# Performance work log

Measured on AMD Instinct MI355X. Metric: run time of the kernel, lower is better.

## Reference

```python
import jax, jax.numpy as jnp
import numpy as np

N_NODES = 50000
N_EDGES = 1600000
IN_CH = 256
LAT = 32
HID = 64
OUT_CH = 256
GAT_H = 32  # GAT hidden dims [32, 32], heads=1


def setup_inputs() -> dict:
    key = jax.random.key(0)
    ks = jax.random.split(key, 30)
    nrm = lambda k, shape, s=0.05: jax.random.normal(k, shape, dtype=jnp.float32) * s
    inp = {}
    inp["x"] = jax.random.normal(ks[0], (N_NODES, IN_CH), dtype=jnp.float32)
    inp["edge_index"] = jax.random.randint(ks[1], (2, N_EDGES), 0, N_NODES)
    # GAT layer 1: IN_CH -> 32 (heads=1), layer 2: 32 -> 32, final linear 32 -> LAT
    inp["W_g1"] = nrm(ks[2], (IN_CH, GAT_H)); inp["as_g1"] = nrm(ks[3], (GAT_H,)); inp["ad_g1"] = nrm(ks[4], (GAT_H,)); inp["b_g1"] = jnp.zeros((GAT_H,), jnp.float32)
    inp["W_g2"] = nrm(ks[5], (GAT_H, GAT_H)); inp["as_g2"] = nrm(ks[6], (GAT_H,)); inp["ad_g2"] = nrm(ks[7], (GAT_H,)); inp["b_g2"] = jnp.zeros((GAT_H,), jnp.float32)
    inp["W_gf"] = nrm(ks[8], (GAT_H, LAT)); inp["b_gf"] = jnp.zeros((LAT,), jnp.float32)
    inp["W_m1"] = nrm(ks[9], (IN_CH, HID)); inp["b_m1"] = jnp.zeros((HID,), jnp.float32); inp["g_m1"] = jnp.ones((HID,), jnp.float32); inp["be_m1"] = jnp.zeros((HID,), jnp.float32)
    inp["W_m2"] = nrm(ks[10], (HID, HID)); inp["b_m2"] = jnp.zeros((HID,), jnp.float32); inp["g_m2"] = jnp.ones((HID,), jnp.float32); inp["be_m2"] = jnp.zeros((HID,), jnp.float32)
    inp["W_m3"] = nrm(ks[11], (HID, LAT)); inp["b_m3"] = jnp.zeros((LAT,), jnp.float32); inp["g_m3"] = jnp.ones((LAT,), jnp.float32); inp["be_m3"] = jnp.zeros((LAT,), jnp.float32)
    # final linear LAT -> OUT_CH + ReLU
    inp["W_f"] = nrm(ks[12], (LAT, OUT_CH)); inp["b_f"] = jnp.zeros((OUT_CH,), jnp.float32)
    return inp


def _bn_relu(h, g, b):
    # BatchNorm1d in training mode: batch stats, biased variance, eps=1e-5
    m = jnp.mean(h, axis=0)
    v = jnp.var(h, axis=0)
    return jax.nn.relu((h - m) * jax.lax.rsqrt(v + 1e-5) * g + b)


def _gat(h_in, src, dst, W, a_s, a_d, b):
    # PyG GATConv (heads=1): edge (src j -> dst i), e = LeakyReLU(a_src.Wx_j + a_dst.Wx_i)
    N = h_in.shape[0]
    h = h_in @ W                                   # [N, F]
    e = jax.nn.leaky_relu((h @ a_s)[src] + (h @ a_d)[dst], 0.2)  # [E]
    m = jax.ops.segment_max(e, dst, num_segments=N)              # scatter-softmax over incoming edges
    ex = jnp.exp(e - m[dst])
    den = jax.ops.segment_sum(ex, dst, num_segments=N)
    alpha = ex / den[dst]
    out = jax.ops.segment_sum(alpha[:, None] * h[src], dst, num_segments=N)
    return out + b


def reference(x, edge_index, W_g1, as_g1, ad_g1, b_g1, W_g2, as_g2, ad_g2, b_g2, W_gf, b_gf, W_m1, b_m1, g_m1, be_m1, W_m2, b_m2, g_m2, be_m2, W_m3, b_m3, g_m3, be_m3, W_f, b_f):
    N = x.shape[0]
    loops = jnp.arange(N)
    src = jnp.concatenate([edge_index[0], loops])  # PyG add_self_loops=True
    dst = jnp.concatenate([edge_index[1], loops])
    r = _bn_relu(x @ W_m1 + b_m1, g_m1, be_m1)
    r = _bn_relu(r @ W_m2 + b_m2, g_m2, be_m2)
    r = _bn_relu(r @ W_m3 + b_m3, g_m3, be_m3)
    # GAT interpolation branch (dropout inactive in eval)
    h = jax.nn.relu(_gat(x, src, dst, W_g1, as_g1, ad_g1, b_g1))
    h = jax.nn.relu(_gat(h, src, dst, W_g2, as_g2, ad_g2, b_g2))
    h = h @ W_gf + b_gf
    # blend with alphas = 0.5 constant vector
    out = 0.5 * r + 0.5 * h
    return jax.nn.relu(out @ W_f + b_f)
```

## Files before the change

kernel.cpp:

```cpp
#include <hip/hip_runtime.h>

#define NNODES 50000
#define NEDGES 1600000
#define NBUCK 196
#define BIN_CH 8192
#define CNT_CH 4096

__device__ __forceinline__ float leaky02(float x) { return x > 0.f ? x : 0.2f * x; }

__device__ __forceinline__ int block_incl_scan(int v, int* sh) {
  int t = threadIdx.x;
  sh[t] = v;
  __syncthreads();
  for (int d = 1; d < 256; d <<= 1) {
    int u = (t >= d) ? sh[t - d] : 0;
    __syncthreads();
    sh[t] += u;
    __syncthreads();
  }
  return sh[t];
}

__global__ __launch_bounds__(256) void k_b0(const int* __restrict__ dst,
                                            int* __restrict__ gcnt, int E) {
  __shared__ int hist[256];
  int t = threadIdx.x;
  hist[t] = 0;
  __syncthreads();
  int base0 = blockIdx.x * CNT_CH;
#pragma unroll
  for (int r = 0; r < CNT_CH / 256; ++r) {
    int idx = base0 + r * 256 + t;
    if (idx < E) atomicAdd(&hist[dst[idx] >> 8], 1);
  }
  __syncthreads();
  if (t < NBUCK && hist[t]) atomicAdd(&gcnt[t], hist[t]);
}

__global__ __launch_bounds__(256) void k_b1(const int* __restrict__ gcnt,
                                            int* __restrict__ base,
                                            int* __restrict__ cursor) {
  __shared__ int sh[256];
  int t = threadIdx.x;
  int v = (t < NBUCK) ? gcnt[t] : 0;
  int incl = block_incl_scan(v, sh);
  if (t < NBUCK) {
    base[t] = incl - v;
    cursor[t] = incl - v;
  }
  if (t == 255) base[NBUCK] = NEDGES;
}

__global__ __launch_bounds__(256) void k_bin(const int* __restrict__ src,
                                             const int* __restrict__ dst,
                                             int* __restrict__ cursor,
                                             unsigned* __restrict__ binned, int E) {
  __shared__ int hist[256];
  __shared__ int scanbuf[256];
  __shared__ int LS[NBUCK + 1];
  __shared__ int cur[256];
  __shared__ int gbase[256];
  __shared__ unsigned stage[BIN_CH];
  int t = threadIdx.x;
  int base0 = blockIdx.x * BIN_CH;
  int cnt = E - base0;
  if (cnt > BIN_CH) cnt = BIN_CH;

  unsigned pk[BIN_CH / 256];
  hist[t] = 0;
  __syncthreads();
#pragma unroll
  for (int r = 0; r < BIN_CH / 256; ++r) {
    int idx = base0 + r * 256 + t;
    if (idx < E) {
      unsigned p = ((unsigned)dst[idx] << 16) | (unsigned)src[idx];
      pk[r] = p;
      atomicAdd(&hist[p >> 24], 1);
    }
  }
  __syncthreads();
  int incl = block_incl_scan(hist[t], scanbuf);
  if (t == 0) LS[0] = 0;
  if (t < NBUCK) LS[t + 1] = incl;
  if (t < NBUCK && hist[t]) gbase[t] = atomicAdd(&cursor[t], hist[t]);
  __syncthreads();
  cur[t] = LS[t < NBUCK ? t : NBUCK];
  __syncthreads();
#pragma unroll
  for (int r = 0; r < BIN_CH / 256; ++r) {
    int idx = base0 + r * 256 + t;
    if (idx < E) {
      unsigned p = pk[r];
      int pos = atomicAdd(&cur[p >> 24], 1);
      stage[pos] = p;
    }
  }
  __syncthreads();
  for (int i = t; i < cnt; i += 256) {
    int lo = 0, hi = NBUCK;
    while (hi - lo > 1) {
      int mid = (lo + hi) >> 1;
      if (i >= LS[mid]) lo = mid; else hi = mid;
    }
    binned[gbase[lo] + (i - LS[lo])] = stage[i];
  }
}

__global__ __launch_bounds__(256) void k_sort(const unsigned* __restrict__ binned,
                                              const int* __restrict__ base,
                                              int* __restrict__ deg,
                                              int* __restrict__ offs,
                                              int* __restrict__ csr) {
  __shared__ int hist[256];
  __shared__ int scanbuf[256];
  __shared__ int cur[256];
  int t = threadIdx.x;
  int b = blockIdx.x;
  int lo = base[b], hi = base[b + 1];
  int node0 = b << 8;
  hist[t] = 0;
  __syncthreads();
  for (int i = lo + t; i < hi; i += 256)
    atomicAdd(&hist[(binned[i] >> 16) & 255], 1);
  __syncthreads();
  int h = hist[t];
  int incl = block_incl_scan(h, scanbuf);
  int excl = incl - h;
  int node = node0 + t;
  if (node < NNODES) {
    deg[node] = h;
    offs[node] = lo + excl;
  }
  cur[t] = lo + excl;
  __syncthreads();
  for (int i = lo + t; i < hi; i += 256) {
    unsigned p = binned[i];
    int pos = atomicAdd(&cur[(p >> 16) & 255], 1);
    csr[pos] = (int)(p & 0xFFFFu);
  }
}

template <int K, int KC, int NC, int TN, int SPLIT, bool BN, bool STATS>
__global__ __launch_bounds__(256) void k_gemm(
    const float* __restrict__ A, const float* __restrict__ scale,
    const float* __restrict__ shift, const float* __restrict__ B0,
    const float* __restrict__ B1, const float* __restrict__ bias0,
    float* __restrict__ out0, float* __restrict__ out1,
    float* __restrict__ gsum, float* __restrict__ gsq, int M) {
  __shared__ float As[128][68];
  __shared__ float Bs[KC][NC];
  const int tid = threadIdx.x;
  const int row0 = blockIdx.x * 128;
  const int cg = tid & 15;
  const int rowg = (tid >> 4) & 15;

  float acc[8][TN];
#pragma unroll
  for (int r = 0; r < 8; ++r)
#pragma unroll
    for (int j = 0; j < TN; ++j) acc[r][j] = 0.f;

  constexpr int KB = KC / 4;
  for (int k0 = 0; k0 < K; k0 += KC) {
#pragma unroll
    for (int it = 0; it < (128 * KB) / 256; ++it) {
      int idx = tid + it * 256;
      int row = idx / KB;
      int kb = idx % KB;
      float4 v = make_float4(0.f, 0.f, 0.f, 0.f);
      int grow = row0 + row;
      if (grow < M) {
        v = *reinterpret_cast<const float4*>(&A[(size_t)grow * K + k0 + kb * 4]);
        if (BN) {
          int kb4 = k0 + kb * 4;
          float4 sc = *reinterpret_cast<const float4*>(&scale[kb4]);
          float4 sf = *reinterpret_cast<const float4*>(&shift[kb4]);
          v.x = fmaxf(v.x * sc.x + sf.x, 0.f);
          v.y = fmaxf(v.y * sc.y + sf.y, 0.f);
          v.z = fmaxf(v.z * sc.z + sf.z, 0.f);
          v.w = fmaxf(v.w * sc.w + sf.w, 0.f);
        }
      }
      *reinterpret_cast<float4*>(&As[row][kb * 4]) = v;
    }
#pragma unroll
    for (int it = 0; it < (KC * SPLIT) / 256; ++it) {
      int idx = tid + it * 256;
      int kk = idx / SPLIT;
      int c = idx % SPLIT;
      Bs[kk][c] = B0[(size_t)(k0 + kk) * SPLIT + c];
    }
    if constexpr (NC > SPLIT) {
      constexpr int W1 = NC - SPLIT;
#pragma unroll
      for (int it = 0; it < (KC * W1) / 256; ++it) {
        int idx = tid + it * 256;
        int kk = idx / W1;
        int c = idx % W1;
        Bs[kk][SPLIT + c] = B1[(size_t)(k0 + kk) * W1 + c];
      }
    }
    __syncthreads();
    for (int kk = 0; kk < KC; kk += 4) {
      float4 a[8];
#pragma unroll
      for (int r = 0; r < 8; ++r)
        a[r] = *reinterpret_cast<const float4*>(&As[rowg + 16 * r][kk]);
      float b[4][TN];
#pragma unroll
      for (int i = 0; i < 4; ++i)
#pragma unroll
        for (int j = 0; j < TN; ++j) b[i][j] = Bs[kk + i][cg * TN + j];
#pragma unroll
      for (int r = 0; r < 8; ++r)
#pragma unroll
        for (int j = 0; j < TN; ++j) {
          acc[r][j] += a[r].x * b[0][j];
          acc[r][j] += a[r].y * b[1][j];
          acc[r][j] += a[r].z * b[2][j];
          acc[r][j] += a[r].w * b[3][j];
        }
    }
    __syncthreads();
  }
  float bias_r[TN];
#pragma unroll
  for (int j = 0; j < TN; ++j) {
    int c = cg * TN + j;
    bias_r[j] = (c < SPLIT) ? bias0[c] : 0.f;
  }
  float cs[TN], cq[TN];
#pragma unroll
  for (int j = 0; j < TN; ++j) { cs[j] = 0.f; cq[j] = 0.f; }
#pragma unroll
  for (int r = 0; r < 8; ++r) {
    int grow = row0 + rowg + 16 * r;
    if (grow < M) {
#pragma unroll
      for (int j = 0; j < TN; ++j) {
        int c = cg * TN + j;
        if (c < SPLIT) {
          float v = acc[r][j] + bias_r[j];
          out0[(size_t)grow * SPLIT + c] = v;
          if (STATS) { cs[j] += v; cq[j] += v * v; }
        } else {
          out1[(size_t)grow * (NC - SPLIT) + (c - SPLIT)] = acc[r][j];
        }
      }
    }
  }
  if constexpr (STATS) {
#pragma unroll
    for (int j = 0; j < TN; ++j) {
      cs[j] += __shfl_xor(cs[j], 16);
      cs[j] += __shfl_xor(cs[j], 32);
      cq[j] += __shfl_xor(cq[j], 16);
      cq[j] += __shfl_xor(cq[j], 32);
    }
    float* red = &Bs[0][0];
    int wave = tid >> 6;
    int lane = tid & 63;
    if (lane < 16) {
#pragma unroll
      for (int j = 0; j < TN; ++j) {
        int c = cg * TN + j;
        if (c < SPLIT) {
          red[wave * 2 * SPLIT + c] = cs[j];
          red[wave * 2 * SPLIT + SPLIT + c] = cq[j];
        }
      }
    }
    __syncthreads();
    if (tid < SPLIT) {
      float s = red[tid] + red[2 * SPLIT + tid] + red[4 * SPLIT + tid] + red[6 * SPLIT + tid];
      atomicAdd(&gsum[tid], s);
    } else if (tid < 2 * SPLIT) {
      int c = tid - SPLIT;
      float q = red[SPLIT + c] + red[3 * SPLIT + c] + red[5 * SPLIT + c] + red[7 * SPLIT + c];
      atomicAdd(&gsq[c], q);
    }
  }
}

__global__ __launch_bounds__(256) void k_sdot(const float* __restrict__ g,
                                              const float* __restrict__ as_,
                                              const float* __restrict__ ad_,
                                              float* __restrict__ sv,
                                              float* __restrict__ dv, int N) {
  int lane = threadIdx.x & 31;
  int row = blockIdx.x * 8 + (threadIdx.x >> 5);
  if (row >= N) return;
  float v = g[(size_t)row * 32 + lane];
  float a = v * as_[lane];
  float b = v * ad_[lane];
#pragma unroll
  for (int w = 16; w >= 1; w >>= 1) {
    a += __shfl_xor(a, w);
    b += __shfl_xor(b, w);
  }
  if (lane == 0) {
    sv[row] = a;
    dv[row] = b;
  }
}

__global__ __launch_bounds__(256) void k_gat_agg(
    const float* __restrict__ h, const float* __restrict__ sv,
    const float* __restrict__ dv, const int* __restrict__ offs,
    const int* __restrict__ deg, const int* __restrict__ csr,
    const float* __restrict__ bias, float* __restrict__ out, int N) {
  int lane = threadIdx.x & 31;
  int node = blockIdx.x * 8 + (threadIdx.x >> 5);
  if (node >= N) return;
  int start = offs[node];
  int cnt = deg[node];
  float di = dv[node];
  float ex0 = __expf(leaky02(sv[node] + di));
  float den = ex0;
  float acc = ex0 * h[(size_t)node * 32 + lane];
  int k = 0;
  for (; k + 8 <= cnt; k += 8) {
    int j0 = csr[start + k + 0], j1 = csr[start + k + 1];
    int j2 = csr[start + k + 2], j3 = csr[start + k + 3];
    int j4 = csr[start + k + 4], j5 = csr[start + k + 5];
    int j6 = csr[start + k + 6], j7 = csr[start + k + 7];
    float s0 = sv[j0], s1 = sv[j1], s2 = sv[j2], s3 = sv[j3];
    float s4 = sv[j4], s5 = sv[j5], s6 = sv[j6], s7 = sv[j7];
    float h0 = h[(size_t)j0 * 32 + lane], h1 = h[(size_t)j1 * 32 + lane];
    float h2 = h[(size_t)j2 * 32 + lane], h3 = h[(size_t)j3 * 32 + lane];
    float h4 = h[(size_t)j4 * 32 + lane], h5 = h[(size_t)j5 * 32 + lane];
    float h6 = h[(size_t)j6 * 32 + lane], h7 = h[(size_t)j7 * 32 + lane];
    float e0 = __expf(leaky02(s0 + di)), e1 = __expf(leaky02(s1 + di));
    float e2 = __expf(leaky02(s2 + di)), e3 = __expf(leaky02(s3 + di));
    float e4 = __expf(leaky02(s4 + di)), e5 = __expf(leaky02(s5 + di));
    float e6 = __expf(leaky02(s6 + di)), e7 = __expf(leaky02(s7 + di));
    den += ((e0 + e1) + (e2 + e3)) + ((e4 + e5) + (e6 + e7));
    acc += e0 * h0 + e1 * h1 + e2 * h2 + e3 * h3;
    acc += e4 * h4 + e5 * h5 + e6 * h6 + e7 * h7;
  }
  for (; k < cnt; ++k) {
    int j = csr[start + k];
    float ex = __expf(leaky02(sv[j] + di));
    den += ex;
    acc += ex * h[(size_t)j * 32 + lane];
  }
  out[(size_t)node * 32 + lane] = fmaxf(acc / den + bias[lane], 0.f);
}

__global__ __launch_bounds__(256) void k_small_gemm_sd(
    const float* __restrict__ hin, const float* __restrict__ W,
    const float* __restrict__ as_, const float* __restrict__ ad_,
    float* __restrict__ gout, float* __restrict__ sv, float* __restrict__ dv,
    int N) {
  __shared__ float Ws[32][32];
  {
    int t = threadIdx.x;
#pragma unroll
    for (int r = 0; r < 4; ++r) {
      int idx = t + r * 256;
      Ws[idx >> 5][idx & 31] = W[idx];
    }
  }
  __syncthreads();
  int lane = threadIdx.x & 31;
  int row = blockIdx.x * 8 + (threadIdx.x >> 5);
  if (row >= N) return;
  float hv = hin[(size_t)row * 32 + lane];
  float acc = 0.f;
#pragma unroll
  for (int k = 0; k < 32; ++k) acc += __shfl(hv, k, 32) * Ws[k][lane];
  gout[(size_t)row * 32 + lane] = acc;
  float a = acc * as_[lane];
  float b = acc * ad_[lane];
#pragma unroll
  for (int w = 16; w >= 1; w >>= 1) {
    a += __shfl_xor(a, w);
    b += __shfl_xor(b, w);
  }
  if (lane == 0) {
    sv[row] = a;
    dv[row] = b;
  }
}

__global__ void k_finalize(const float* __restrict__ sum, const float* __restrict__ sumsq,
                           const float* __restrict__ gamma, const float* __restrict__ beta,
                           float* __restrict__ scale, float* __restrict__ shift, int NC,
                           float invM) {
  int c = threadIdx.x;
  if (c < NC) {
    float mean = sum[c] * invM;
    float var = sumsq[c] * invM - mean * mean;
    float rs = rsqrtf(var + 1e-5f);
    float sc = rs * gamma[c];
    scale[c] = sc;
    shift[c] = beta[c] - mean * sc;
  }
}

__global__ __launch_bounds__(256) void k_final2(
    const float* __restrict__ mlp3, const float* __restrict__ sc3,
    const float* __restrict__ sh3, const float* __restrict__ h2,
    const float* __restrict__ Wgf, const float* __restrict__ bgf,
    const float* __restrict__ Wf, const float* __restrict__ bf,
    float* __restrict__ out, int N) {
  __shared__ float WfS[32 * 256];
  __shared__ float Bl[64][36];
  __shared__ float WgfS[32][33];
  __shared__ float colS[3][32];
  const int t = threadIdx.x;
  const int row0 = blockIdx.x * 64;

  {
    const float4* src = reinterpret_cast<const float4*>(Wf);
    float4* dst = reinterpret_cast<float4*>(WfS);
#pragma unroll
    for (int r = 0; r < 8; ++r) dst[t + r * 256] = src[t + r * 256];
  }
#pragma unroll
  for (int r = 0; r < 4; ++r) {
    int idx = t + r * 256;
    WgfS[idx >> 5][idx & 31] = Wgf[idx];
  }
  if (t < 32) {
    colS[0][t] = sc3[t];
    colS[1][t] = sh3[t];
    colS[2][t] = bgf[t];
  }
#pragma unroll
  for (int r = 0; r < 2; ++r) {
    int idx = t + r * 256;
    int row = idx >> 3;
    int k4 = idx & 7;
    int grow = row0 + row;
    float4 v = make_float4(0.f, 0.f, 0.f, 0.f);
    if (grow < N) v = *reinterpret_cast<const float4*>(&h2[(size_t)grow * 32 + k4 * 4]);
    *reinterpret_cast<float4*>(&Bl[row][k4 * 4]) = v;
  }
  __syncthreads();

  const int col = t & 31;
  const int rb = t >> 5;
  float w[32];
#pragma unroll
  for (int k = 0; k < 32; ++k) w[k] = WgfS[k][col];
  float bl[8];
#pragma unroll
  for (int r = 0; r < 8; ++r) {
    int row = rb + 8 * r;
    float a = colS[2][col];
#pragma unroll
    for (int k4 = 0; k4 < 8; ++k4) {
      float4 hv = *reinterpret_cast<const float4*>(&Bl[row][k4 * 4]);
      a += hv.x * w[k4 * 4 + 0] + hv.y * w[k4 * 4 + 1] +
           hv.z * w[k4 * 4 + 2] + hv.w * w[k4 * 4 + 3];
    }
    int grow = row0 + row;
    float pre = (grow < N) ? mlp3[(size_t)grow * 32 + col] : 0.f;
    float rv = fmaxf(pre * colS[0][col] + colS[1][col], 0.f);
    bl[r] = 0.5f * rv + 0.5f * a;
  }
  __syncthreads();
#pragma unroll
  for (int r = 0; r < 8; ++r) Bl[rb + 8 * r][col] = bl[r];
  __syncthreads();

  const int cg = t & 31;
  const int rowg = t >> 5;
  const float4* Wf4 = reinterpret_cast<const float4*>(WfS);
  float4 acc0[8], acc1[8];
#pragma unroll
  for (int r = 0; r < 8; ++r) {
    acc0[r] = make_float4(0.f, 0.f, 0.f, 0.f);
    acc1[r] = make_float4(0.f, 0.f, 0.f, 0.f);
  }
  for (int k = 0; k < 32; k += 4) {
    float4 a[8];
#pragma unroll
    for (int r = 0; r < 8; ++r)
      a[r] = *reinterpret_cast<const float4*>(&Bl[rowg + 8 * r][k]);
    float4 b0[4], b1[4];
#pragma unroll
    for (int i = 0; i < 4; ++i) {
      b0[i] = Wf4[(k + i) * 64 + cg];
      b1[i] = Wf4[(k + i) * 64 + cg + 32];
    }
#pragma unroll
    for (int r = 0; r < 8; ++r) {
      float av[4] = {a[r].x, a[r].y, a[r].z, a[r].w};
#pragma unroll
      for (int i = 0; i < 4; ++i) {
        acc0[r].x += av[i] * b0[i].x;
        acc0[r].y += av[i] * b0[i].y;
        acc0[r].z += av[i] * b0[i].z;
        acc0[r].w += av[i] * b0[i].w;
        acc1[r].x += av[i] * b1[i].x;
        acc1[r].y += av[i] * b1[i].y;
        acc1[r].z += av[i] * b1[i].z;
        acc1[r].w += av[i] * b1[i].w;
      }
    }
  }
  float4 bfA = reinterpret_cast<const float4*>(bf)[cg];
  float4 bfB = reinterpret_cast<const float4*>(bf)[cg + 32];
  float4* out4 = reinterpret_cast<float4*>(out);
#pragma unroll
  for (int r = 0; r < 8; ++r) {
    int grow = row0 + rowg + 8 * r;
    if (grow < N) {
      float4 o0 = acc0[r], o1 = acc1[r];
      o0.x = fmaxf(o0.x + bfA.x, 0.f); o0.y = fmaxf(o0.y + bfA.y, 0.f);
      o0.z = fmaxf(o0.z + bfA.z, 0.f); o0.w = fmaxf(o0.w + bfA.w, 0.f);
      o1.x = fmaxf(o1.x + bfB.x, 0.f); o1.y = fmaxf(o1.y + bfB.y, 0.f);
      o1.z = fmaxf(o1.z + bfB.z, 0.f); o1.w = fmaxf(o1.w + bfB.w, 0.f);
      out4[(size_t)grow * 64 + cg] = o0;
      out4[(size_t)grow * 64 + cg + 32] = o1;
    }
  }
}

extern "C" void kernel_launch(void* const* d_in, const int* in_sizes, int n_in,
                              void* d_out, int out_size, void* d_ws, size_t ws_size,
                              hipStream_t stream) {
  const float* x = (const float*)d_in[0];
  const int* edge = (const int*)d_in[1];
  const float* W_g1 = (const float*)d_in[2];
  const float* as_g1 = (const float*)d_in[3];
  const float* ad_g1 = (const float*)d_in[4];
  const float* b_g1 = (const float*)d_in[5];
  const float* W_g2 = (const float*)d_in[6];
  const float* as_g2 = (const float*)d_in[7];
  const float* ad_g2 = (const float*)d_in[8];
  const float* b_g2 = (const float*)d_in[9];
  const float* W_gf = (const float*)d_in[10];
  const float* b_gf = (const float*)d_in[11];
  const float* W_m1 = (const float*)d_in[12];
  const float* b_m1 = (const float*)d_in[13];
  const float* g_m1 = (const float*)d_in[14];
  const float* be_m1 = (const float*)d_in[15];
  const float* W_m2 = (const float*)d_in[16];
  const float* b_m2 = (const float*)d_in[17];
  const float* g_m2 = (const float*)d_in[18];
  const float* be_m2 = (const float*)d_in[19];
  const float* W_m3 = (const float*)d_in[20];
  const float* b_m3 = (const float*)d_in[21];
  const float* g_m3 = (const float*)d_in[22];
  const float* be_m3 = (const float*)d_in[23];
  const float* W_f = (const float*)d_in[24];
  const float* b_f = (const float*)d_in[25];
  float* out = (float*)d_out;

  const int N = NNODES, E = NEDGES;
  const int* esrc = edge;
  const int* edst = edge + E;

  float* ws = (float*)d_ws;
  float* g1 = ws;
  float* mlp1 = g1 + (size_t)N * 32;
  float* mlp2 = mlp1 + (size_t)N * 64;
  float* mlp3 = mlp2 + (size_t)N * 64;
  float* h1 = mlp3 + (size_t)N * 32;
  float* g2 = h1 + (size_t)N * 32;
  float* h2 = g2 + (size_t)N * 32;
  float* s1 = h2 + (size_t)N * 32;
  float* d1 = s1 + N;
  float* s2 = d1 + N;
  float* d2 = s2 + N;
  float* stats = d2 + N;
  float* sum1 = stats, *sq1 = stats + 64;
  float* sum2 = stats + 128, *sq2 = stats + 192;
  float* sum3 = stats + 256, *sq3 = stats + 288;
  float* scsh = stats + 320;
  float* sc1 = scsh, *sh1 = scsh + 64;
  float* sc2 = scsh + 128, *sh2 = scsh + 192;
  float* sc3 = scsh + 256, *sh3 = scsh + 288;
  int* ip = (int*)(scsh + 320);
  int* gcnt = ip;
  int* base = gcnt + 256;
  int* cursor = base + 256;
  int* deg = cursor + 256;
  int* offs = deg + N;
  int* csr = offs + N;
  unsigned* binned = (unsigned*)mlp2;

  hipMemsetAsync(gcnt, 0, 256 * sizeof(int), stream);
  hipMemsetAsync(stats, 0, 320 * sizeof(float), stream);

  k_b0<<<(E + CNT_CH - 1) / CNT_CH, 256, 0, stream>>>(edst, gcnt, E);
  k_b1<<<1, 256, 0, stream>>>(gcnt, base, cursor);
  k_bin<<<(E + BIN_CH - 1) / BIN_CH, 256, 0, stream>>>(esrc, edst, cursor, binned, E);
  k_sort<<<NBUCK, 256, 0, stream>>>(binned, base, deg, offs, csr);

  const int GB = (N + 127) / 128;

  k_gemm<256, 64, 96, 6, 64, false, true><<<GB, 256, 0, stream>>>(
      x, nullptr, nullptr, W_m1, W_g1, b_m1, mlp1, g1, sum1, sq1, N);
  k_sdot<<<(N + 7) / 8, 256, 0, stream>>>(g1, as_g1, ad_g1, s1, d1, N);
  k_finalize<<<1, 64, 0, stream>>>(sum1, sq1, g_m1, be_m1, sc1, sh1, 64, 1.f / N);
  k_gat_agg<<<(N + 7) / 8, 256, 0, stream>>>(g1, s1, d1, offs, deg, csr, b_g1, h1, N);

  k_gemm<64, 64, 64, 4, 64, true, true><<<GB, 256, 0, stream>>>(
      mlp1, sc1, sh1, W_m2, nullptr, b_m2, mlp2, nullptr, sum2, sq2, N);
  k_finalize<<<1, 64, 0, stream>>>(sum2, sq2, g_m2, be_m2, sc2, sh2, 64, 1.f / N);

  k_small_gemm_sd<<<(N + 7) / 8, 256, 0, stream>>>(h1, W_g2, as_g2, ad_g2, g2, s2, d2, N);
  k_gat_agg<<<(N + 7) / 8, 256, 0, stream>>>(g2, s2, d2, offs, deg, csr, b_g2, h2, N);

  k_gemm<64, 64, 32, 2, 32, true, true><<<GB, 256, 0, stream>>>(
      mlp2, sc2, sh2, W_m3, nullptr, b_m3, mlp3, nullptr, sum3, sq3, N);
  k_finalize<<<1, 32, 0, stream>>>(sum3, sq3, g_m3, be_m3, sc3, sh3, 32, 1.f / N);

  k_final2<<<(N + 63) / 64, 256, 0, stream>>>(mlp3, sc3, sh3, h2, W_gf, b_gf,
                                              W_f, b_f, out, N);
}
```

Baseline: 440.7 us.

## Fold BN finalize into consumers, simplify binning scatter, vectorize GEMM B loads

Removes the three single-block BatchNorm finalize launches: each consuming GEMM and the final kernel now compute scale and shift from the accumulated sums in shared memory. The edge-binning kernel drops its local shared-memory staging and binary search and scatters packed edges straight to global positions from per-block atomics, with a smaller chunk size. The GEMM weight tile loads become float4, the first GEMM uses a smaller K chunk, and the A tile loses its row padding. This saves launch and serialization overhead, but the direct scatter is less coalesced, and the unpadded A tile may raise LDS bank conflicts.

```diff
diff --git a/kernel.cpp b/kernel.cpp
--- a/kernel.cpp
+++ b/kernel.cpp
@@ -3,7 +3,7 @@
 #define NNODES 50000
 #define NEDGES 1600000
 #define NBUCK 196
-#define BIN_CH 8192
+#define BIN_CH 4096
 #define CNT_CH 4096
 
 __device__ __forceinline__ float leaky02(float x) { return x > 0.f ? x : 0.2f * x; }
@@ -56,16 +56,9 @@
                                              int* __restrict__ cursor,
                                              unsigned* __restrict__ binned, int E) {
   __shared__ int hist[256];
-  __shared__ int scanbuf[256];
-  __shared__ int LS[NBUCK + 1];
   __shared__ int cur[256];
-  __shared__ int gbase[256];
-  __shared__ unsigned stage[BIN_CH];
   int t = threadIdx.x;
   int base0 = blockIdx.x * BIN_CH;
-  int cnt = E - base0;
-  if (cnt > BIN_CH) cnt = BIN_CH;
-
   unsigned pk[BIN_CH / 256];
   hist[t] = 0;
   __syncthreads();
@@ -79,12 +72,7 @@
     }
   }
   __syncthreads();
-  int incl = block_incl_scan(hist[t], scanbuf);
-  if (t == 0) LS[0] = 0;
-  if (t < NBUCK) LS[t + 1] = incl;
-  if (t < NBUCK && hist[t]) gbase[t] = atomicAdd(&cursor[t], hist[t]);
-  __syncthreads();
-  cur[t] = LS[t < NBUCK ? t : NBUCK];
+  if (t < NBUCK && hist[t]) cur[t] = atomicAdd(&cursor[t], hist[t]);
   __syncthreads();
 #pragma unroll
   for (int r = 0; r < BIN_CH / 256; ++r) {
@@ -92,17 +80,8 @@
     if (idx < E) {
       unsigned p = pk[r];
       int pos = atomicAdd(&cur[p >> 24], 1);
-      stage[pos] = p;
-    }
-  }
-  __syncthreads();
-  for (int i = t; i < cnt; i += 256) {
-    int lo = 0, hi = NBUCK;
-    while (hi - lo > 1) {
-      int mid = (lo + hi) >> 1;
-      if (i >= LS[mid]) lo = mid; else hi = mid;
-    }
-    binned[gbase[lo] + (i - LS[lo])] = stage[i];
+      binned[pos] = p;
+    }
   }
 }
 
@@ -142,17 +121,33 @@
 
 template <int K, int KC, int NC, int TN, int SPLIT, bool BN, bool STATS>
 __global__ __launch_bounds__(256) void k_gemm(
-    const float* __restrict__ A, const float* __restrict__ scale,
-    const float* __restrict__ shift, const float* __restrict__ B0,
-    const float* __restrict__ B1, const float* __restrict__ bias0,
+    const float* __restrict__ A, const float* __restrict__ bn_sum,
+    const float* __restrict__ bn_sq, const float* __restrict__ bn_gamma,
+    const float* __restrict__ bn_beta, float invM,
+    const float* __restrict__ B0, const float* __restrict__ B1,
+    const float* __restrict__ bias0,
     float* __restrict__ out0, float* __restrict__ out1,
     float* __restrict__ gsum, float* __restrict__ gsq, int M) {
-  __shared__ float As[128][68];
-  __shared__ float Bs[KC][NC];
+  __shared__ float As[128 * KC];
+  __shared__ float Bs[KC * NC];
+  __shared__ float scS[BN ? K : 4];
+  __shared__ float shS[BN ? K : 4];
   const int tid = threadIdx.x;
   const int row0 = blockIdx.x * 128;
   const int cg = tid & 15;
   const int rowg = (tid >> 4) & 15;
+
+  if constexpr (BN) {
+    if (tid < K) {
+      float mean = bn_sum[tid] * invM;
+      float var = bn_sq[tid] * invM - mean * mean;
+      float rs = rsqrtf(var + 1e-5f);
+      float sc = rs * bn_gamma[tid];
+      scS[tid] = sc;
+      shS[tid] = bn_beta[tid] - mean * sc;
+    }
+    __syncthreads();
+  }
 
   float acc[8][TN];
 #pragma unroll
@@ -171,33 +166,39 @@
       int grow = row0 + row;
       if (grow < M) {
         v = *reinterpret_cast<const float4*>(&A[(size_t)grow * K + k0 + kb * 4]);
-        if (BN) {
+        if constexpr (BN) {
           int kb4 = k0 + kb * 4;
-          float4 sc = *reinterpret_cast<const float4*>(&scale[kb4]);
-          float4 sf = *reinterpret_cast<const float4*>(&shift[kb4]);
+          float4 sc = *reinterpret_cast<const float4*>(&scS[kb4]);
+          float4 sf = *reinterpret_cast<const float4*>(&shS[kb4]);
           v.x = fmaxf(v.x * sc.x + sf.x, 0.f);
           v.y = fmaxf(v.y * sc.y + sf.y, 0.f);
           v.z = fmaxf(v.z * sc.z + sf.z, 0.f);
           v.w = fmaxf(v.w * sc.w + sf.w, 0.f);
         }
       }
-      *reinterpret_cast<float4*>(&As[row][kb * 4]) = v;
-    }
-#pragma unroll
-    for (int it = 0; it < (KC * SPLIT) / 256; ++it) {
-      int idx = tid + it * 256;
-      int kk = idx / SPLIT;
-      int c = idx % SPLIT;
-      Bs[kk][c] = B0[(size_t)(k0 + kk) * SPLIT + c];
+      *reinterpret_cast<float4*>(&As[row * KC + kb * 4]) = v;
+    }
+    {
+      constexpr int KB0 = SPLIT / 4;
+#pragma unroll
+      for (int it = 0; it < (KC * KB0) / 256; ++it) {
+        int idx = tid + it * 256;
+        int kk = idx / KB0;
+        int cb = idx % KB0;
+        float4 v = *reinterpret_cast<const float4*>(&B0[(size_t)(k0 + kk) * SPLIT + cb * 4]);
+        *reinterpret_cast<float4*>(&Bs[kk * NC + cb * 4]) = v;
+      }
     }
     if constexpr (NC > SPLIT) {
       constexpr int W1 = NC - SPLIT;
-#pragma unroll
-      for (int it = 0; it < (KC * W1) / 256; ++it) {
+      constexpr int KB1 = W1 / 4;
+#pragma unroll
+      for (int it = 0; it < (KC * KB1) / 256; ++it) {
         int idx = tid + it * 256;
-        int kk = idx / W1;
-        int c = idx % W1;
-        Bs[kk][SPLIT + c] = B1[(size_t)(k0 + kk) * W1 + c];
+        int kk = idx / KB1;
+        int cb = idx % KB1;
+        float4 v = *reinterpret_cast<const float4*>(&B1[(size_t)(k0 + kk) * W1 + cb * 4]);
+        *reinterpret_cast<float4*>(&Bs[kk * NC + SPLIT + cb * 4]) = v;
       }
     }
     __syncthreads();
@@ -205,12 +206,12 @@
       float4 a[8];
 #pragma unroll
       for (int r = 0; r < 8; ++r)
-        a[r] = *reinterpret_cast<const float4*>(&As[rowg + 16 * r][kk]);
+        a[r] = *reinterpret_cast<const float4*>(&As[(rowg + 16 * r) * KC + kk]);
       float b[4][TN];
 #pragma unroll
       for (int i = 0; i < 4; ++i)
 #pragma unroll
-        for (int j = 0; j < TN; ++j) b[i][j] = Bs[kk + i][cg * TN + j];
+        for (int j = 0; j < TN; ++j) b[i][j] = Bs[(kk + i) * NC + cg * TN + j];
 #pragma unroll
       for (int r = 0; r < 8; ++r)
 #pragma unroll
@@ -257,7 +258,7 @@
       cq[j] += __shfl_xor(cq[j], 16);
       cq[j] += __shfl_xor(cq[j], 32);
     }
-    float* red = &Bs[0][0];
+    float* red = Bs;
     int wave = tid >> 6;
     int lane = tid & 63;
     if (lane < 16) {
@@ -383,24 +384,10 @@
   }
 }
 
-__global__ void k_finalize(const float* __restrict__ sum, const float* __restrict__ sumsq,
-                           const float* __restrict__ gamma, const float* __restrict__ beta,
-                           float* __restrict__ scale, float* __restrict__ shift, int NC,
-                           float invM) {
-  int c = threadIdx.x;
-  if (c < NC) {
-    float mean = sum[c] * invM;
-    float var = sumsq[c] * invM - mean * mean;
-    float rs = rsqrtf(var + 1e-5f);
-    float sc = rs * gamma[c];
-    scale[c] = sc;
-    shift[c] = beta[c] - mean * sc;
-  }
-}
-
 __global__ __launch_bounds__(256) void k_final2(
-    const float* __restrict__ mlp3, const float* __restrict__ sc3,
-    const float* __restrict__ sh3, const float* __restrict__ h2,
+    const float* __restrict__ mlp3, const float* __restrict__ sum3,
+    const float* __restrict__ sq3, const float* __restrict__ g3,
+    const float* __restrict__ be3, float invM, const float* __restrict__ h2,
     const float* __restrict__ Wgf, const float* __restrict__ bgf,
     const float* __restrict__ Wf, const float* __restrict__ bf,
     float* __restrict__ out, int N) {
@@ -423,8 +410,12 @@
     WgfS[idx >> 5][idx & 31] = Wgf[idx];
   }
   if (t < 32) {
-    colS[0][t] = sc3[t];
-    colS[1][t] = sh3[t];
+    float mean = sum3[t] * invM;
+    float var = sq3[t] * invM - mean * mean;
+    float rs = rsqrtf(var + 1e-5f);
+    float sc = rs * g3[t];
+    colS[0][t] = sc;
+    colS[1][t] = be3[t] - mean * sc;
     colS[2][t] = bgf[t];
   }
 #pragma unroll
@@ -551,6 +542,7 @@
   float* out = (float*)d_out;
 
   const int N = NNODES, E = NEDGES;
+  const float invM = 1.f / N;
   const int* esrc = edge;
   const int* edst = edge + E;
 
@@ -570,11 +562,7 @@
   float* sum1 = stats, *sq1 = stats + 64;
   float* sum2 = stats + 128, *sq2 = stats + 192;
   float* sum3 = stats + 256, *sq3 = stats + 288;
-  float* scsh = stats + 320;
-  float* sc1 = scsh, *sh1 = scsh + 64;
-  float* sc2 = scsh + 128, *sh2 = scsh + 192;
-  float* sc3 = scsh + 256, *sh3 = scsh + 288;
-  int* ip = (int*)(scsh + 320);
+  int* ip = (int*)(stats + 384);
   int* gcnt = ip;
   int* base = gcnt + 256;
   int* cursor = base + 256;
@@ -584,7 +572,7 @@
   unsigned* binned = (unsigned*)mlp2;
 
   hipMemsetAsync(gcnt, 0, 256 * sizeof(int), stream);
-  hipMemsetAsync(stats, 0, 320 * sizeof(float), stream);
+  hipMemsetAsync(stats, 0, 384 * sizeof(float), stream);
 
   k_b0<<<(E + CNT_CH - 1) / CNT_CH, 256, 0, stream>>>(edst, gcnt, E);
   k_b1<<<1, 256, 0, stream>>>(gcnt, base, cursor);
@@ -593,23 +581,23 @@
 
   const int GB = (N + 127) / 128;
 
-  k_gemm<256, 64, 96, 6, 64, false, true><<<GB, 256, 0, stream>>>(
-      x, nullptr, nullptr, W_m1, W_g1, b_m1, mlp1, g1, sum1, sq1, N);
+  k_gemm<256, 32, 96, 6, 64, false, true><<<GB, 256, 0, stream>>>(
+      x, nullptr, nullptr, nullptr, nullptr, invM, W_m1, W_g1, b_m1,
+      mlp1, g1, sum1, sq1, N);
   k_sdot<<<(N + 7) / 8, 256, 0, stream>>>(g1, as_g1, ad_g1, s1, d1, N);
-  k_finalize<<<1, 64, 0, stream>>>(sum1, sq1, g_m1, be_m1, sc1, sh1, 64, 1.f / N);
   k_gat_agg<<<(N + 7) / 8, 256, 0, stream>>>(g1, s1, d1, offs, deg, csr, b_g1, h1, N);
 
   k_gemm<64, 64, 64, 4, 64, true, true><<<GB, 256, 0, stream>>>(
-      mlp1, sc1, sh1, W_m2, nullptr, b_m2, mlp2, nullptr, sum2, sq2, N);
-  k_finalize<<<1, 64, 0, stream>>>(sum2, sq2, g_m2, be_m2, sc2, sh2, 64, 1.f / N);
+      mlp1, sum1, sq1, g_m1, be_m1, invM, W_m2, nullptr, b_m2,
+      mlp2, nullptr, sum2, sq2, N);
 
   k_small_gemm_sd<<<(N + 7) / 8, 256, 0, stream>>>(h1, W_g2, as_g2, ad_g2, g2, s2, d2, N);
   k_gat_agg<<<(N + 7) / 8, 256, 0, stream>>>(g2, s2, d2, offs, deg, csr, b_g2, h2, N);
 
   k_gemm<64, 64, 32, 2, 32, true, true><<<GB, 256, 0, stream>>>(
-      mlp2, sc2, sh2, W_m3, nullptr, b_m3, mlp3, nullptr, sum3, sq3, N);
-  k_finalize<<<1, 32, 0, stream>>>(sum3, sq3, g_m3, be_m3, sc3, sh3, 32, 1.f / N);
-
-  k_final2<<<(N + 63) / 64, 256, 0, stream>>>(mlp3, sc3, sh3, h2, W_gf, b_gf,
-                                              W_f, b_f, out, N);
-}
+      mlp2, sum2, sq2, g_m2, be_m2, invM, W_m3, nullptr, b_m3,
+      mlp3, nullptr, sum3, sq3, N);
+
+  k_final2<<<(N + 63) / 64, 256, 0, stream>>>(mlp3, sum3, sq3, g_m3, be_m3, invM,
+                                              h2, W_gf, b_gf, W_f, b_f, out, N);
+}
```

After: 417.9 us. 1.05x faster.
